# Performance work log

Hardware: AMD Instinct MI355X
Metric: run time of the kernel (lower is better)

The kernel has to match this reference:

```python
import jax, jax.numpy as jnp
from jax import lax
import numpy as np

EPS = 1e-5
K = 16
NUM_GROUP = 128
D = 384
HEADS = 6
DEPTH = 4
BETA = 0.25

def gelu(x):
    return jax.nn.gelu(x, approximate=False)

def linear(x, w, b):
    return x @ w.T + b

def layer_norm(x, g, b):
    mu = x.mean(-1, keepdims=True)
    var = x.var(-1, keepdims=True)
    return (x - mu) / jnp.sqrt(var + EPS) * g + b

def group_norm(x, gamma, beta, groups):
    B, C = x.shape[0], x.shape[1]
    sp = x.shape[2:]
    xg = x.reshape((B, groups, C // groups) + sp)
    axes = tuple(range(2, xg.ndim))
    mu = xg.mean(axes, keepdims=True)
    var = xg.var(axes, keepdims=True)
    xg = (xg - mu) / jnp.sqrt(var + EPS)
    x = xg.reshape((B, C) + sp)
    shp = (1, C) + (1,) * len(sp)
    return x * gamma.reshape(shp) + beta.reshape(shp)

def knn_idx(q, kp, k):
    # q [B,Nq,3], kp [B,Nk,3] -> idx [B,Nq,k] of k nearest keys
    d = jnp.sum(q * q, -1)[:, :, None] - 2.0 * jnp.einsum('bqd,bkd->bqk', q, kp) + jnp.sum(kp * kp, -1)[:, None, :]
    _, idx = lax.top_k(-d, k)
    return idx

def graph_feature(coor_q, x_q, coor_k, x_k, k):
    # coor [B,3,N], x [B,C,N] -> [B,2C,Nq,k]
    idx = knn_idx(coor_q.transpose(0, 2, 1), coor_k.transpose(0, 2, 1), k)
    feat = jax.vmap(lambda a, i: a[:, i])(x_k, idx)  # [B,C,Nq,k]
    xq = x_q[:, :, :, None]
    return jnp.concatenate([feat - xq, jnp.broadcast_to(xq, feat.shape)], axis=1)

def fps_indices(xyz, m):
    # farthest point sampling, start at index 0 (matches pointnet2)
    B, N, _ = xyz.shape
    def body(carry, _):
        dist, far = carry
        c = jnp.take_along_axis(xyz, far[:, None, None], axis=1)
        d = jnp.sum((xyz - c) ** 2, -1)
        dist = jnp.minimum(dist, d)
        return (dist, jnp.argmax(dist, -1).astype(jnp.int32)), far
    init = (jnp.full((B, N), 1e10, xyz.dtype), jnp.zeros((B,), jnp.int32))
    _, idxs = lax.scan(body, init, None, length=m)
    return idxs.T  # [B,m]

def gather_ch(x, idx):
    return jax.vmap(lambda a, i: a[:, i])(x, idx)

def conv1x1_2d(x, w):
    return jnp.einsum('oc,bcnk->bonk', w, x)

def conv1x1_1d(x, w, b):
    return jnp.einsum('oc,bcn->bon', w, x) + b[None, :, None]

def linear_resize(x, out_len):
    # F.interpolate(mode='linear', align_corners=False) along axis 1 of [B,N,D]
    n = x.shape[1]
    pos = (jnp.arange(out_len, dtype=x.dtype) + 0.5) * (n / out_len) - 0.5
    pos = jnp.clip(pos, 0.0, n - 1.0)
    i0 = jnp.floor(pos).astype(jnp.int32)
    i1 = jnp.minimum(i0 + 1, n - 1)
    w = (pos - i0.astype(x.dtype))[None, :, None]
    return x[:, i0] * (1.0 - w) + x[:, i1] * w

def vq(z, cb, beta):
    d = jnp.sum(z * z, -1, keepdims=True) - 2.0 * (z @ cb.T) + jnp.sum(cb * cb, -1)
    eidx = jnp.argmin(d, -1)
    q = cb[eidx]
    loss = jnp.mean((lax.stop_gradient(z) - q) ** 2) + beta * jnp.mean((z - lax.stop_gradient(q)) ** 2)
    q_st = z + lax.stop_gradient(q - z)  # straight-through
    return q_st, loss, eidx

def forward_core(xyz, it_w, it_b, g1_w, g1_g, g1_bt, g2_w, g2_g, g2_bt, g3_w, g3_g, g3_bt, g4_w, g4_g, g4_bt, pe_w1, pe_b1, pe_w2, pe_b2, ip_w1, ip_b1, ip_w2, ip_b2, ln1_g, ln1_b, qkv_w, qkv_b, o_w, o_b, ln2_g, ln2_b, m1_w, m1_b, m2_w, m2_b, pyr_w1, pyr_b1, pyr_g1, pyr_bt1, pyr_w2, pyr_b2, pyr_g2, pyr_bt2, fus_w, fus_b, cb0, cb1, cb2):
    B = xyz.shape[0]
    x = xyz.transpose(0, 2, 1)  # [B,7,N]
    coor, normal, plane = x[:, :3], x[:, 3:6], x[:, 6:7]
    f = conv1x1_1d(coor, it_w, it_b)  # [B,8,N]

    def edge_conv(cq, fq, ck, fk, w, g, bt, groups):
        h = graph_feature(cq, fq, ck, fk, K)
        h = conv1x1_2d(h, w)
        h = group_norm(h, g, bt, groups)
        h = jnp.where(h > 0, h, 0.2 * h)  # LeakyReLU(0.2)
        return h.max(axis=-1)

    f = edge_conv(coor, f, coor, f, g1_w, g1_g, g1_bt, 4)  # [B,32,N]
    idx = fps_indices(coor.transpose(0, 2, 1), NUM_GROUP)
    coor_q, normal_q, plane_q, f_q = gather_ch(coor, idx), gather_ch(normal, idx), gather_ch(plane, idx), gather_ch(f, idx)
    f = edge_conv(coor_q, f_q, coor, f, g2_w, g2_g, g2_bt, 4)  # [B,64,128]
    coor, normal, plane = coor_q, normal_q, plane_q
    f = edge_conv(coor, f, coor, f, g3_w, g3_g, g3_bt, 4)  # [B,64,128]
    idx = fps_indices(coor.transpose(0, 2, 1), NUM_GROUP)
    coor_q, normal_q, plane_q, f_q = gather_ch(coor, idx), gather_ch(normal, idx), gather_ch(plane, idx), gather_ch(f, idx)
    f = edge_conv(coor_q, f_q, coor, f, g4_w, g4_g, g4_bt, 4)  # [B,128,128]
    coor = coor_q.transpose(0, 2, 1)  # [B,128,3]
    f = f.transpose(0, 2, 1)          # [B,128,128]

    pe = linear(gelu(linear(coor, pe_w1, pe_b1)), pe_w2, pe_b2)
    h = linear(gelu(linear(f, ip_w1, ip_b1)), ip_w2, ip_b2)
    t = h + pe
    hd = D // HEADS
    scale = 1.0 / np.sqrt(hd)
    N = t.shape[1]
    for l in range(DEPTH):
        hn = layer_norm(t, ln1_g[l], ln1_b[l])
        qkv = hn @ qkv_w[l] + qkv_b[l]
        q, k_, v = jnp.split(qkv, 3, axis=-1)
        q = q.reshape(B, N, HEADS, hd)
        k_ = k_.reshape(B, N, HEADS, hd)
        v = v.reshape(B, N, HEADS, hd)
        att = jax.nn.softmax(jnp.einsum('bqhd,bkhd->bhqk', q, k_) * scale, axis=-1)
        o = jnp.einsum('bhqk,bkhd->bqhd', att, v).reshape(B, N, D)
        t = t + o @ o_w[l] + o_b[l]
        hn = layer_norm(t, ln2_g[l], ln2_b[l])
        t = t + gelu(hn @ m1_w[l] + m1_b[l]) @ m2_w[l] + m2_b[l]

    base = t  # [B,128,384]
    cbs = (cb0, cb1, cb2)
    outs, losses, idxs = [], [], []
    prev = None
    for level in range(3):
        res = max(base.shape[1] // (2 ** level), 8)
        if res == base.shape[1]:
            lf = base
        else:
            # adaptive_avg_pool1d with evenly dividing bins == reshape-mean
            lf = base.reshape(B, res, base.shape[1] // res, D).mean(2)
        c = lf.transpose(0, 2, 1)
        c = gelu(group_norm(conv1x1_1d(c, pyr_w1[level], pyr_b1[level]), pyr_g1[level], pyr_bt1[level], 8))
        c = gelu(group_norm(conv1x1_1d(c, pyr_w2[level], pyr_b2[level]), pyr_g2[level], pyr_bt2[level], 8))
        proc = c.transpose(0, 2, 1)
        if level > 0:
            pu = prev if prev.shape[1] == res else linear_resize(prev, res)
            proc = gelu(linear(jnp.concatenate([proc, pu], axis=-1), fus_w[level - 1], fus_b[level - 1]))
        q_st, loss, eidx = vq(proc, cbs[level], BETA)
        outs.append(q_st)
        losses.append(loss)
        idxs.append(eidx)
        prev = q_st
    return outs, losses, idxs

def setup_inputs():
    key = jax.random.key(0)
    cnt = [0]
    def nrm(shape, s=0.02):
        cnt[0] += 1
        return jax.random.normal(jax.random.fold_in(key, cnt[0]), shape, jnp.float32) * s
    L = 4
    inp = {}
    inp['xyz'] = nrm((8, 4096, 7), 1.0)
    inp['it_w'] = nrm((8, 3), 0.3)
    inp['it_b'] = jnp.zeros((8,), jnp.float32)
    inp['g1_w'] = nrm((32, 16), 0.1); inp['g1_g'] = jnp.ones((32,)); inp['g1_bt'] = jnp.zeros((32,))
    inp['g2_w'] = nrm((64, 64), 0.1); inp['g2_g'] = jnp.ones((64,)); inp['g2_bt'] = jnp.zeros((64,))
    inp['g3_w'] = nrm((64, 128), 0.1); inp['g3_g'] = jnp.ones((64,)); inp['g3_bt'] = jnp.zeros((64,))
    inp['g4_w'] = nrm((128, 128), 0.1); inp['g4_g'] = jnp.ones((128,)); inp['g4_bt'] = jnp.zeros((128,))
    inp['pe_w1'] = nrm((128, 3), 0.3); inp['pe_b1'] = jnp.zeros((128,))
    inp['pe_w2'] = nrm((D, 128), 0.05); inp['pe_b2'] = jnp.zeros((D,))
    inp['ip_w1'] = nrm((512, 128), 0.05); inp['ip_b1'] = jnp.zeros((512,))
    inp['ip_w2'] = nrm((D, 512), 0.03); inp['ip_b2'] = jnp.zeros((D,))
    inp['ln1_g'] = jnp.ones((L, D)); inp['ln1_b'] = jnp.zeros((L, D))
    inp['qkv_w'] = nrm((L, D, 3 * D)); inp['qkv_b'] = jnp.zeros((L, 3 * D))
    inp['o_w'] = nrm((L, D, D)); inp['o_b'] = jnp.zeros((L, D))
    inp['ln2_g'] = jnp.ones((L, D)); inp['ln2_b'] = jnp.zeros((L, D))
    inp['m1_w'] = nrm((L, D, 4 * D)); inp['m1_b'] = jnp.zeros((L, 4 * D))
    inp['m2_w'] = nrm((L, 4 * D, D)); inp['m2_b'] = jnp.zeros((L, D))
    inp['pyr_w1'] = nrm((3, 2 * D, D), 0.03); inp['pyr_b1'] = jnp.zeros((3, 2 * D))
    inp['pyr_g1'] = jnp.ones((3, 2 * D)); inp['pyr_bt1'] = jnp.zeros((3, 2 * D))
    inp['pyr_w2'] = nrm((3, D, 2 * D), 0.03); inp['pyr_b2'] = jnp.zeros((3, D))
    inp['pyr_g2'] = jnp.ones((3, D)); inp['pyr_bt2'] = jnp.zeros((3, D))
    inp['fus_w'] = nrm((2, D, 2 * D), 0.03); inp['fus_b'] = jnp.zeros((2, D))
    inp['cb0'] = nrm((8192, D), 0.5)
    inp['cb1'] = nrm((4096, D), 0.5)
    inp['cb2'] = nrm((2048, D), 0.5)
    return inp

def reference(xyz, it_w, it_b, g1_w, g1_g, g1_bt, g2_w, g2_g, g2_bt, g3_w, g3_g, g3_bt, g4_w, g4_g, g4_bt, pe_w1, pe_b1, pe_w2, pe_b2, ip_w1, ip_b1, ip_w2, ip_b2, ln1_g, ln1_b, qkv_w, qkv_b, o_w, o_b, ln2_g, ln2_b, m1_w, m1_b, m2_w, m2_b, pyr_w1, pyr_b1, pyr_g1, pyr_bt1, pyr_w2, pyr_b2, pyr_g2, pyr_bt2, fus_w, fus_b, cb0, cb1, cb2):
    outs, losses, idxs = forward_core(xyz, it_w, it_b, g1_w, g1_g, g1_bt, g2_w, g2_g, g2_bt, g3_w, g3_g, g3_bt, g4_w, g4_g, g4_bt, pe_w1, pe_b1, pe_w2, pe_b2, ip_w1, ip_b1, ip_w2, ip_b2, ln1_g, ln1_b, qkv_w, qkv_b, o_w, o_b, ln2_g, ln2_b, m1_w, m1_b, m2_w, m2_b, pyr_w1, pyr_b1, pyr_g1, pyr_bt1, pyr_w2, pyr_b2, pyr_g2, pyr_bt2, fus_w, fus_b, cb0, cb1, cb2)
    # concat quantized features of the 3 levels (128+64+32 tokens), total VQ loss, per-level indices
    return (jnp.concatenate(outs, axis=1), losses[0] + losses[1] + losses[2], idxs[0], idxs[1], idxs[2])
```

## Files before the change

### kernel.cpp

```cpp
#include <hip/hip_runtime.h>
#include <math.h>

#define EPSF 1e-5f

__device__ __forceinline__ float geluf(float x){
  return 0.5f*x*(1.0f + erff(x*0.70710678118654752440f));
}

typedef __attribute__((ext_vector_type(8))) short bf16x8;
typedef __attribute__((ext_vector_type(4))) float f32x4;

__device__ __forceinline__ void split_rne(float x, short& h, short& l){
  union{float f; unsigned u;} xu; xu.f = x;
  unsigned lsb = (xu.u >> 16) & 1u;
  unsigned hb = (xu.u + 0x7fffu + lsb) >> 16;
  union{unsigned u; float f;} hf; hf.u = hb << 16;
  float lof = x - hf.f;
  union{float f; unsigned u;} lu; lu.f = lof;
  unsigned lsb2 = (lu.u >> 16) & 1u;
  unsigned lb = (lu.u + 0x7fffu + lsb2) >> 16;
  h = (short)hb;
  l = (short)lb;
}


__global__ void extract_coor(const float* __restrict__ xyz, float* __restrict__ coor, int B, int N){
  int i = blockIdx.x*blockDim.x + threadIdx.x;
  if(i >= B*3*N) return;
  int n = i % N; int c = (i/N)%3; int b = i/(3*N);
  coor[i] = xyz[((size_t)b*N + n)*7 + c];
}

__global__ void init_feat(const float* __restrict__ xyz, const float* __restrict__ w,
                          const float* __restrict__ bias, float* __restrict__ f, int B, int N){
  int i = blockIdx.x*blockDim.x + threadIdx.x;
  if(i >= B*8*N) return;
  int n = i % N; int c = (i/N)%8; int b = i/(8*N);
  const float* p = xyz + ((size_t)b*N + n)*7;
  f[i] = w[c*3+0]*p[0] + w[c*3+1]*p[1] + w[c*3+2]*p[2] + bias[c];
}

__global__ void transpose_cn(const float* __restrict__ src, float* __restrict__ dst, int B, int C, int N){
  int i = blockIdx.x*blockDim.x + threadIdx.x;
  if(i >= B*C*N) return;
  int c = i % C; int n = (i/C)%N; int b = i/(C*N);
  dst[i] = src[((size_t)b*C + c)*N + n];
}

__global__ void gather_ch_kernel(const float* __restrict__ src, const int* __restrict__ idx,
                                 float* __restrict__ dst, int B, int C, int N, int M){
  int i = blockIdx.x*blockDim.x + threadIdx.x;
  if(i >= B*C*M) return;
  int m = i % M; int c = (i/M)%C; int b = i/(C*M);
  dst[i] = src[((size_t)b*C + c)*N + idx[b*M + m]];
// ... 2 lines not shown
__global__ void split_planes(const float* __restrict__ src, short* __restrict__ hi,
                             short* __restrict__ lo, int n4){
  int i = blockIdx.x*blockDim.x + threadIdx.x;
  if(i >= n4) return;
  float4 v = *(const float4*)(src + (size_t)i*4);
  short h0,h1,h2,h3,l0,l1,l2,l3;
  split_rne(v.x,h0,l0); split_rne(v.y,h1,l1); split_rne(v.z,h2,l2); split_rne(v.w,h3,l3);
  unsigned hw0 = ((unsigned)(unsigned short)h0) | (((unsigned)(unsigned short)h1)<<16);
  unsigned hw1 = ((unsigned)(unsigned short)h2) | (((unsigned)(unsigned short)h3)<<16);
  unsigned lw0 = ((unsigned)(unsigned short)l0) | (((unsigned)(unsigned short)l1)<<16);
  unsigned lw1 = ((unsigned)(unsigned short)l2) | (((unsigned)(unsigned short)l3)<<16);
  ((unsigned*)hi)[(size_t)i*2+0] = hw0; ((unsigned*)hi)[(size_t)i*2+1] = hw1;
  ((unsigned*)lo)[(size_t)i*2+0] = lw0; ((unsigned*)lo)[(size_t)i*2+1] = lw1;
}

#define KNN_K 16
template<int NKMAX, int NT>
__global__ __launch_bounds__(NT) void knn_kernel(const float* __restrict__ Q, const float* __restrict__ Kp,
                                                 int* __restrict__ idxout, int B, int Nq, int Nk){
  constexpr int NW = NT/64;
  __shared__ float4 sk[NKMAX];
  __shared__ float scd[NW][64];
  __shared__ int   sci[NW][64];
  __shared__ int   scnt[NW];
  int qi0 = blockIdx.x*NW;
  int b = qi0 / Nq;
  const float* kb = Kp + (size_t)b*3*Nk;
  if(threadIdx.x < NW) scnt[threadIdx.x] = 0;
  for(int n=threadIdx.x; n<Nk; n+=NT){
    float x = kb[n], y = kb[Nk+n], z = kb[2*Nk+n];
    sk[n] = make_float4(x, y, z, fmaf(x,x, fmaf(y,y, z*z)));
  }
  __syncthreads();
  int wave = threadIdx.x >> 6;
  int lane = threadIdx.x & 63;
  int n_q = qi0 + wave - b*Nq;
  float nqx = -2.0f*Q[((size_t)b*3+0)*Nq + n_q];
  float nqy = -2.0f*Q[((size_t)b*3+1)*Nq + n_q];
  float nqz = -2.0f*Q[((size_t)b*3+2)*Nq + n_q];

  float mind = INFINITY;
  for(int n=lane; n<Nk; n+=64){
    float4 k4 = sk[n];
    float d = fmaf(nqx, k4.x, fmaf(nqy, k4.y, fmaf(nqz, k4.z, k4.w)));
    mind = fminf(mind, d);
  }
  {
    float v = mind;
    #pragma unroll
    for(int k=2;k<=64;k<<=1){
      #pragma unroll
      for(int j=k>>1;j>=1;j>>=1){
        float ov = __shfl_xor(v, j, 64);
        bool lower = (lane & j)==0;
        bool asc = (lane & k)==0;
        float mn = fminf(v,ov), mx = fmaxf(v,ov);
        v = (lower==asc) ? mn : mx;
      }
    }
    mind = v;
  }
  float tau = __shfl(mind, 15, 64);

  for(int n=lane; n<Nk; n+=64){
    float4 k4 = sk[n];
    float d = fmaf(nqx, k4.x, fmaf(nqy, k4.y, fmaf(nqz, k4.z, k4.w)));
    if(d <= tau){
      int slot = atomicAdd(&scnt[wave], 1);
      if(slot < 64){ scd[wave][slot] = d; sci[wave][slot] = n; }
    }
  }
  __syncthreads();
  int cnt = scnt[wave];

  int* orow = idxout + ((size_t)b*Nq + n_q)*KNN_K;
  if(cnt <= 64){
    float d = (lane < cnt) ? scd[wave][lane] : INFINITY;
    int  id = (lane < cnt) ? sci[wave][lane] : 0x7fffffff;
    #pragma unroll
    for(int k=2;k<=64;k<<=1){
      #pragma unroll
      for(int j=k>>1;j>=1;j>>=1){
        float od = __shfl_xor(d, j, 64);
        int oi = __shfl_xor(id, j, 64);
        bool lower = (lane & j)==0;
        bool asc = (lane & k)==0;
        bool otherSmaller = (od < d) || (od==d && oi < id);
        if((lower==asc) == otherSmaller){ d = od; id = oi; }
      }
    }
    if(lane < KNN_K) orow[lane] = id;
  } else {
    float bd[KNN_K]; int bi2[KNN_K];
    #pragma unroll
    for(int j=0;j<KNN_K;j++){ bd[j]=INFINITY; bi2[j]=0x7fffffff; }
    float curmax = INFINITY;
    for(int n=lane; n<Nk; n+=64){
      float4 k4 = sk[n];
      float d = fmaf(nqx, k4.x, fmaf(nqy, k4.y, fmaf(nqz, k4.z, k4.w)));
      if(d < curmax){
        int pm = 0; float md = bd[0]; int mi = bi2[0];
        #pragma unroll
        for(int j=1;j<KNN_K;j++){
          if(bd[j] > md || (bd[j]==md && bi2[j] > mi)){ md=bd[j]; mi=bi2[j]; pm=j; }
        }
        #pragma unroll
        for(int j=0;j<KNN_K;j++){ if(j==pm){ bd[j]=d; bi2[j]=n; } }
        float m2 = -INFINITY;
        #pragma unroll
        for(int j=0;j<KNN_K;j++) m2 = fmaxf(m2, bd[j]);
        curmax = m2;
      }
    }
    for(int t=0;t<KNN_K;t++){
      float ld = bd[0]; int li_ = bi2[0];
      #pragma unroll
      for(int j=1;j<KNN_K;j++){
        if(bd[j] < ld || (bd[j]==ld && bi2[j] < li_)){ ld=bd[j]; li_=bi2[j]; }
      }
      float wd = ld; int wi = li_;
      #pragma unroll
      for(int m=1;m<64;m<<=1){
        float od = __shfl_xor(wd, m, 64);
        int oi = __shfl_xor(wi, m, 64);
        if(od < wd || (od==wd && oi < wi)){ wd=od; wi=oi; }
      }
      if(ld==wd && li_==wi){
        #pragma unroll
        for(int j=0;j<KNN_K;j++){ if(bd[j]==wd && bi2[j]==wi){ bd[j]=INFINITY; bi2[j]=0x7fffffff; } }
      }
      if(lane==0) orow[t] = wi;
    }
  }
}

template<int NMAX, int PPT, int NT>
__global__ __launch_bounds__(NT) void fps_kernel(const float* __restrict__ coor, int* __restrict__ out,
                                                 int N, int M){
  __shared__ float skx[NMAX], sky[NMAX], skz[NMAX];
  __shared__ unsigned long long swk[NT/64];
  __shared__ int gidx;
  constexpr int NW = NT/64;
  int b = blockIdx.x;
  int tid = threadIdx.x;
  int lane = tid & 63, wid = tid >> 6;
  const float* cx = coor + (size_t)b*3*N;
// ... 299 lines not shown
    }
  };
  auto stageB = [&](){
    #pragma unroll
    for(int v8=0; v8<2; v8++){
      bf16x8 h, l;
      #pragma unroll
      for(int j=0;j<8;j++){
        short th, tl;
        split_rne(breg[v8*8+j], th, tl);
        h[j] = th; l[j] = tl;
      }
      *(bf16x8*)&sBhi[bc_][bkq + v8*8] = h;
      *(bf16x8*)&sBlo[bc_][bkq + v8*8] = l;
    }
  };

  loadA(0); loadB(0);
  int nk = K >> 6;
  for(int ki=0; ki<nk; ki++){
    stageA(ki*64); stageB();
    __syncthreads();
    if(ki+1 < nk){ loadA((ki+1)*64); loadB((ki+1)*64); }
    #pragma unroll
    for(int half=0; half<2; half++){
      bf16x8 ah[2], al[2], bh[2], bl[2];
      #pragma unroll
      for(int m=0;m<2;m++){
        int arow = wm*32 + m*16 + rr;
        ah[m] = *(bf16x8*)&sAhi[arow][half*32 + g*8];
// ... 269 lines not shown
  }
}

__global__ void loss_kernel(const float* __restrict__ lossacc, float* __restrict__ out){
  float m0 = lossacc[0]/(8.0f*128.0f*384.0f);
  float m1 = lossacc[1]/(8.0f*64.0f*384.0f);
  float m2 = lossacc[2]/(8.0f*32.0f*384.0f);
  out[0] = (m0 + 0.25f*m0) + (m1 + 0.25f*m1) + (m2 + 0.25f*m2);
}


extern "C" void kernel_launch(void* const* d_in, const int* in_sizes, int n_in,
                              void* d_out, int out_size, void* d_ws, size_t ws_size,
                              hipStream_t stream)
{
  (void)in_sizes; (void)n_in; (void)out_size; (void)ws_size;
  const float* xyz   = (const float*)d_in[0];
  const float* it_w  = (const float*)d_in[1];
  const float* it_b  = (const float*)d_in[2];
  const float* g1_w  = (const float*)d_in[3];
  const float* g1_g  = (const float*)d_in[4];
  const float* g1_bt = (const float*)d_in[5];
  const float* g2_w  = (const float*)d_in[6];
  const float* g2_g  = (const float*)d_in[7];
  const float* g2_bt = (const float*)d_in[8];
  const float* g3_w  = (const float*)d_in[9];
  const float* g3_g  = (const float*)d_in[10];
  const float* g3_bt = (const float*)d_in[11];
  const float* g4_w  = (const float*)d_in[12];
  const float* g4_g  = (const float*)d_in[13];
  const float* g4_bt = (const float*)d_in[14];
// ... 61 lines not shown
  constexpr size_t OFF_LF    = OFF_MID + (size_t)1024*1536;
  constexpr size_t OFF_C1    = OFF_LF + (size_t)512*384;
  constexpr size_t OFF_C2    = OFF_C1 + (size_t)1024*768;
  constexpr size_t OFF_CAT   = OFF_C2 + (size_t)1024*384;
  constexpr size_t OFF_PROC  = OFF_CAT + (size_t)512*768;
  constexpr size_t OFF_KEYS  = OFF_PROC + (size_t)512*384;
  constexpr size_t OFF_LNMR  = OFF_KEYS + 3584;
  constexpr size_t OFF_CBSQ  = OFF_LNMR + 2048;
  constexpr size_t OFF_PART  = OFF_CBSQ + 14336;
  constexpr size_t OFF_MR    = OFF_PART + 32768;
  constexpr size_t OFF_LOSS  = OFF_MR + 64;
  constexpr size_t OFF_ZHI   = OFF_LOSS + 64;
  constexpr size_t OFF_ZLO   = OFF_ZHI + 196608;
  constexpr size_t OFF_CBHI  = OFF_ZLO + 196608;
  constexpr size_t OFF_CBLO  = OFF_CBHI + 2752512;

  float* coor0 = ws + OFF_COOR0;
  float* f0    = ws + OFF_F0;
  float* f1    = ws + OFF_F1;
  int*   idx1  = (int*)(ws + OFF_IDX1);
  int*   fps1  = (int*)(ws + OFF_FPS1);
  float* coor1 = ws + OFF_COOR1;
  float* f1q   = ws + OFF_F1Q;
  int*   idx2  = (int*)(ws + OFF_IDX2);
  float* f2    = ws + OFF_F2;
  int*   idx3  = (int*)(ws + OFF_IDX3);
  float* f3    = ws + OFF_F3;
  int*   fps2  = (int*)(ws + OFF_FPS2);
  float* coor2 = ws + OFF_COOR2;
  float* f3q   = ws + OFF_F3Q;
// ... 9 lines not shown
  float* lfb   = ws + OFF_LF;
  float* c1b   = ws + OFF_C1;
  float* c2b   = ws + OFF_C2;
  float* catb  = ws + OFF_CAT;
  float* procb = ws + OFF_PROC;
  unsigned long long* keys = (unsigned long long*)(ws + OFF_KEYS);
  float* lnst  = ws + OFF_LNMR;
  float* cbsq  = ws + OFF_CBSQ;
  float* part  = ws + OFF_PART;
  float* mr    = ws + OFF_MR;
  float* lossa = ws + OFF_LOSS;
  short* zhi   = (short*)(ws + OFF_ZHI);
  short* zlo   = (short*)(ws + OFF_ZLO);
  short* cbhi  = (short*)(ws + OFF_CBHI);
  short* cblo  = (short*)(ws + OFF_CBLO);

  auto cdiv = [](int a, int b){ return (a+b-1)/b; };
  auto gemm_full = [&](const float* A, const float* Bm, const float* bias, float* C,
                       int M, int N, int K, int BT, int act, int addto,
                       const float* lnmr, const float* lng, const float* lnb){
    if(((K & 63) == 0) && ((N & 63) == 0) && ((M & 63) == 0)){
      dim3 g(N/64, M/64);
      gemm_mfma<<<g, 256, 0, stream>>>(A, Bm, bias, C, M, N, K, BT, act, addto, lnmr, lng, lnb);
    } else {
      dim3 g(N/64, M/64), blk(128);
      gemm64<<<g, blk, 0, stream>>>(A, Bm, bias, C, M, N, K, BT, act, addto);
    }
  };
  auto gemm = [&](const float* A, const float* Bm, const float* bias, float* C,
                  int M, int N, int K, int BT, int act, int addto){
    gemm_full(A, Bm, bias, C, M, N, K, BT, act, addto, nullptr, nullptr, nullptr);
  };

  hipMemsetAsync(lossa, 0, 8*sizeof(float), stream);
  hipMemsetAsync(keys, 0xFF, 1792*sizeof(unsigned long long), stream);

  extract_coor<<<cdiv(B_*3*N0,256),256,0,stream>>>(xyz, coor0, B_, N0);
  init_feat<<<cdiv(B_*8*N0,256),256,0,stream>>>(xyz, it_w, it_b, f0, B_, N0);

  split_planes<<<cdiv(8192*384/4,256),256,0,stream>>>(cb0, cbhi, cblo, 8192*384/4);
  split_planes<<<cdiv(4096*384/4,256),256,0,stream>>>(cb1, cbhi + (size_t)8192*384, cblo + (size_t)8192*384, 4096*384/4);
  split_planes<<<cdiv(2048*384/4,256),256,0,stream>>>(cb2, cbhi + (size_t)12288*384, cblo + (size_t)12288*384, 2048*384/4);
  cbsq_kernel<<<cdiv(8192,256),256,0,stream>>>(cb0, cbsq, 8192);
  cbsq_kernel<<<cdiv(4096,256),256,0,stream>>>(cb1, cbsq+8192, 4096);
  cbsq_kernel<<<cdiv(2048,256),256,0,stream>>>(cb2, cbsq+12288, 2048);

  knn_kernel<4096,512><<<B_*N0/8,512,0,stream>>>(coor0, coor0, idx1, B_, N0, N0);
  ec_main<8,32><<<B_*32*N0/256,256,0,stream>>>(f0, f0, idx1, g1_w, f1, part, N0, N0);
  ec_reduce<<<32,256,0,stream>>>(part, mr, 32*N0/256, 1.0f/(8.0f*N0*16.0f));
  ec_norm<<<cdiv(B_*32*N0,256),256,0,stream>>>(f1, mr, g1_g, g1_bt, N0, 32, B_*32*N0);

  fps_kernel<4096,8,512><<<B_,512,0,stream>>>(coor0, fps1, N0, M0);
  gather_ch_kernel<<<cdiv(B_*3*M0,256),256,0,stream>>>(coor0, fps1, coor1, B_, 3, N0, M0);
  gather_ch_kernel<<<cdiv(B_*32*M0,256),256,0,stream>>>(f1, fps1, f1q, B_, 32, N0, M0);

  knn_kernel<4096,512><<<B_*M0/8,512,0,stream>>>(coor1, coor0, idx2, B_, M0, N0);
  ec_main<32,64><<<B_*64*M0/256,256,0,stream>>>(f1q, f1, idx2, g2_w, f2, part, M0, N0);
  ec_reduce<<<32,256,0,stream>>>(part, mr, 64*M0/256, 1.0f/(16.0f*M0*16.0f));
  ec_norm<<<cdiv(B_*64*M0,256),256,0,stream>>>(f2, mr, g2_g, g2_bt, M0, 64, B_*64*M0);

  knn_kernel<128,512><<<B_*M0/8,512,0,stream>>>(coor1, coor1, idx3, B_, M0, M0);
  ec_main<64,64><<<B_*64*M0/256,256,0,stream>>>(f2, f2, idx3, g3_w, f3, part, M0, M0);
  ec_reduce<<<32,256,0,stream>>>(part, mr, 64*M0/256, 1.0f/(16.0f*M0*16.0f));
  ec_norm<<<cdiv(B_*64*M0,256),256,0,stream>>>(f3, mr, g3_g, g3_bt, M0, 64, B_*64*M0);

  fps_kernel<128,1,128><<<B_,128,0,stream>>>(coor1, fps2, M0, M0);
  gather_ch_kernel<<<cdiv(B_*3*M0,256),256,0,stream>>>(coor1, fps2, coor2, B_, 3, M0, M0);
  gather_ch_kernel<<<cdiv(B_*64*M0,256),256,0,stream>>>(f3, fps2, f3q, B_, 64, M0, M0);

  knn_kernel<128,512><<<B_*M0/8,512,0,stream>>>(coor2, coor1, idx4, B_, M0, M0);
  ec_main<64,128><<<B_*128*M0/256,256,0,stream>>>(f3q, f3, idx4, g4_w, f4, part, M0, M0);
  ec_reduce<<<32,256,0,stream>>>(part, mr, 128*M0/256, 1.0f/(32.0f*M0*16.0f));
  ec_norm<<<cdiv(B_*128*M0,256),256,0,stream>>>(f4, mr, g4_g, g4_bt, M0, 128, B_*128*M0);

  transpose_cn<<<cdiv(B_*3*M0,256),256,0,stream>>>(coor2, coorT, B_, 3, M0);
  transpose_cn<<<cdiv(B_*128*M0,256),256,0,stream>>>(f4, fT, B_, 128, M0);

  gemm(coorT, pe_w1, pe_b1, tmp, 1024, 128, 3, 1, 1, 0);
  gemm(tmp, pe_w2, pe_b2, tbuf, 1024, 384, 128, 1, 0, 0);
  gemm(fT, ip_w1, ip_b1, tmp, 1024, 512, 128, 1, 1, 0);
  gemm(tmp, ip_w2, ip_b2, tbuf, 1024, 384, 512, 1, 0, 1);

  for(int l=0;l<4;l++){
    ln_stats<<<256,256,0,stream>>>(tbuf, lnst, 384);
    gemm_full(tbuf, qkv_w + (size_t)l*384*1152, qkv_b + l*1152, qkvb, 1024, 1152, 384, 0, 0, 0,
              lnst, ln1_g + l*384, ln1_b + l*384);
    attn_kernel<<<48,128,0,stream>>>(qkvb, attb);
    gemm(attb, o_w + (size_t)l*384*384, o_b + l*384, tbuf, 1024, 384, 384, 0, 0, 1);
    ln_stats<<<256,256,0,stream>>>(tbuf, lnst, 384);
    gemm_full(tbuf, m1_w + (size_t)l*384*1536, m1_b + l*1536, midb, 1024, 1536, 384, 0, 1, 0,
              lnst, ln2_g + l*384, ln2_b + l*384);
    gemm(midb, m2_w + (size_t)l*1536*384, m2_b + l*384, tbuf, 1024, 384, 1536, 0, 0, 1);
  }

  const float* cbs[3] = {cb0, cb1, cb2};
  const int ncodes[3] = {8192, 4096, 2048};
  const int cboff[3]  = {0, 8192, 12288};
  const int keyoff[3] = {0, 1024, 1536};
  const int rowoffs[3] = {0, 128, 192};
  const size_t OUT0 = (size_t)8*224*384;
  float* idxouts[3] = { out + OUT0 + 1, out + OUT0 + 1 + 1024, out + OUT0 + 1 + 1536 };

  for(int lv=0; lv<3; ++lv){
    int res = 128 >> lv;
    int rows = 8*res;
    const float* lf;
    if(lv==0){ lf = tbuf; }
    else {
      pool_kernel<<<cdiv(rows*384,256),256,0,stream>>>(tbuf, lfb, B_, res, 1<<lv);
      lf = lfb;
    }
    gemm(lf, pyr_w1 + (size_t)lv*768*384, pyr_b1 + lv*768, c1b, rows, 768, 384, 1, 0, 0);
    gn_gelu_kernel<<<64,256,0,stream>>>(c1b, pyr_g1 + lv*768, pyr_bt1 + lv*768, res, 768, 96);
    gemm(c1b, pyr_w2 + (size_t)lv*384*768, pyr_b2 + lv*384, c2b, rows, 384, 768, 1, 0, 0);
    gn_gelu_kernel<<<64,256,0,stream>>>(c2b, pyr_g2 + lv*384, pyr_bt2 + lv*384, res, 384, 48);
    const float* z = c2b;
    if(lv > 0){
      pu_cat_kernel<<<cdiv(rows*768,256),256,0,stream>>>(c2b, out, catb, B_, res, rowoffs[lv-1]);
      gemm(catb, fus_w + (size_t)(lv-1)*384*768, fus_b + (lv-1)*384, procb, rows, 384, 768, 1, 1, 0);
      z = procb;
    }
    split_planes<<<cdiv(rows*384/4,256),256,0,stream>>>(z, zhi, zlo, rows*384/4);
    gemm_vq<<<dim3(ncodes[lv]/64, rows/64), 256, 0, stream>>>(zhi, zlo,
        cbhi + (size_t)cboff[lv]*384, cblo + (size_t)cboff[lv]*384,
        cbsq + cboff[lv], keys + keyoff[lv], rows, ncodes[lv], 384);
    vq_out_kernel<<<rows,128,0,stream>>>(z, keys + keyoff[lv], cbs[lv], out, lossa + lv, res,
                                         rowoffs[lv], idxouts[lv]);
  }

  loss_kernel<<<1,1,0,stream>>>(lossa, out + OUT0);
}
```

Measured before the change: 1.813 ms.

## Pre-split weights into bf16 hi/lo planes, pair kNN queries per wave, fuse init kernels

All dense weights are transposed and split once per call into bf16 hi/lo planes in the workspace. A new MFMA GEMM then reads these planes directly instead of converting fp32 weights inside every tile. The kNN kernel now handles two queries per wave so each shared-memory key read serves two distance computations. The coordinate-extract and initial-feature kernels are merged into one launch. The price is extra preprocessing launches and workspace on every call, with a fallback to the old GEMM path when the workspace is too small.

```diff
diff --git a/kernel.cpp b/kernel.cpp
--- a/kernel.cpp
+++ b/kernel.cpp
@@ -24,20 +24,20 @@
 }
 
 
-__global__ void extract_coor(const float* __restrict__ xyz, float* __restrict__ coor, int B, int N){
+__global__ void init_pts(const float* __restrict__ xyz, const float* __restrict__ w,
+                         const float* __restrict__ bias, float* __restrict__ coor,
+                         float* __restrict__ f, int B, int N){
   int i = blockIdx.x*blockDim.x + threadIdx.x;
-  if(i >= B*3*N) return;
-  int n = i % N; int c = (i/N)%3; int b = i/(3*N);
-  coor[i] = xyz[((size_t)b*N + n)*7 + c];
-}
-
-__global__ void init_feat(const float* __restrict__ xyz, const float* __restrict__ w,
-                          const float* __restrict__ bias, float* __restrict__ f, int B, int N){
-  int i = blockIdx.x*blockDim.x + threadIdx.x;
-  if(i >= B*8*N) return;
-  int n = i % N; int c = (i/N)%8; int b = i/(8*N);
-  const float* p = xyz + ((size_t)b*N + n)*7;
-  f[i] = w[c*3+0]*p[0] + w[c*3+1]*p[1] + w[c*3+2]*p[2] + bias[c];
+  if(i >= B*N) return;
+  int n = i % N; int b = i / N;
+  const float* p = xyz + (size_t)i*7;
+  float x = p[0], y = p[1], z = p[2];
+  coor[((size_t)b*3+0)*N+n] = x;
+  coor[((size_t)b*3+1)*N+n] = y;
+  coor[((size_t)b*3+2)*N+n] = z;
+  #pragma unroll
+  for(int c=0;c<8;c++)
+    f[((size_t)b*8+c)*N+n] = w[c*3+0]*x + w[c*3+1]*y + w[c*3+2]*z + bias[c];
 }
 
 __global__ void transpose_cn(const float* __restrict__ src, float* __restrict__ dst, int B, int C, int N){
@@ -70,19 +70,40 @@
   ((unsigned*)lo)[(size_t)i*2+0] = lw0; ((unsigned*)lo)[(size_t)i*2+1] = lw1;
 }
 
+__global__ __launch_bounds__(256) void transpose_split(const float* __restrict__ src,
+    short* __restrict__ hi, short* __restrict__ lo, int K, int N){
+  __shared__ float tile[32][33];
+  int bn = blockIdx.x*32, bk = blockIdx.y*32;
+  int tx = threadIdx.x & 31, ty = threadIdx.x >> 5;
+  #pragma unroll
+  for(int i=ty; i<32; i+=8){
+    int k = bk+i, n = bn+tx;
+    tile[i][tx] = (k<K && n<N) ? src[(size_t)k*N+n] : 0.f;
+  }
+  __syncthreads();
+  #pragma unroll
+  for(int i=ty; i<32; i+=8){
+    int n = bn+i, k = bk+tx;
+    if(n<N && k<K){
+      short h,l; split_rne(tile[tx][i], h, l);
+      hi[(size_t)n*K+k] = h; lo[(size_t)n*K+k] = l;
+    }
+  }
+}
+
 #define KNN_K 16
 template<int NKMAX, int NT>
-__global__ __launch_bounds__(NT) void knn_kernel(const float* __restrict__ Q, const float* __restrict__ Kp,
-                                                 int* __restrict__ idxout, int B, int Nq, int Nk){
+__global__ __launch_bounds__(NT) void knn2q_kernel(const float* __restrict__ Q, const float* __restrict__ Kp,
+                                                   int* __restrict__ idxout, int B, int Nq, int Nk){
   constexpr int NW = NT/64;
   __shared__ float4 sk[NKMAX];
-  __shared__ float scd[NW][64];
-  __shared__ int   sci[NW][64];
-  __shared__ int   scnt[NW];
-  int qi0 = blockIdx.x*NW;
-  int b = qi0 / Nq;
+  __shared__ float scd[NW][2][64];
+  __shared__ int   sci[NW][2][64];
+  __shared__ int   scnt[NW][2];
+  int qb = blockIdx.x*(NW*2);
+  int b = qb / Nq;
   const float* kb = Kp + (size_t)b*3*Nk;
-  if(threadIdx.x < NW) scnt[threadIdx.x] = 0;
+  if(threadIdx.x < NW*2) ((int*)scnt)[threadIdx.x] = 0;
   for(int n=threadIdx.x; n<Nk; n+=NT){
     float x = kb[n], y = kb[Nk+n], z = kb[2*Nk+n];
     sk[n] = make_float4(x, y, z, fmaf(x,x, fmaf(y,y, z*z)));
@@ -90,102 +111,119 @@
   __syncthreads();
   int wave = threadIdx.x >> 6;
   int lane = threadIdx.x & 63;
-  int n_q = qi0 + wave - b*Nq;
-  float nqx = -2.0f*Q[((size_t)b*3+0)*Nq + n_q];
-  float nqy = -2.0f*Q[((size_t)b*3+1)*Nq + n_q];
-  float nqz = -2.0f*Q[((size_t)b*3+2)*Nq + n_q];
-
-  float mind = INFINITY;
+  int nq0 = qb + wave*2 - b*Nq;
+  float q0x = -2.0f*Q[((size_t)b*3+0)*Nq + nq0];
+  float q0y = -2.0f*Q[((size_t)b*3+1)*Nq + nq0];
+  float q0z = -2.0f*Q[((size_t)b*3+2)*Nq + nq0];
+  float q1x = -2.0f*Q[((size_t)b*3+0)*Nq + nq0+1];
+  float q1y = -2.0f*Q[((size_t)b*3+1)*Nq + nq0+1];
+  float q1z = -2.0f*Q[((size_t)b*3+2)*Nq + nq0+1];
+
+  float mind0 = INFINITY, mind1 = INFINITY;
   for(int n=lane; n<Nk; n+=64){
     float4 k4 = sk[n];
-    float d = fmaf(nqx, k4.x, fmaf(nqy, k4.y, fmaf(nqz, k4.z, k4.w)));
-    mind = fminf(mind, d);
+    float d0 = fmaf(q0x, k4.x, fmaf(q0y, k4.y, fmaf(q0z, k4.z, k4.w)));
+    float d1 = fmaf(q1x, k4.x, fmaf(q1y, k4.y, fmaf(q1z, k4.z, k4.w)));
+    mind0 = fminf(mind0, d0);
+    mind1 = fminf(mind1, d1);
   }
   {
-    float v = mind;
+    float v0 = mind0, v1 = mind1;
     #pragma unroll
     for(int k=2;k<=64;k<<=1){
       #pragma unroll
       for(int j=k>>1;j>=1;j>>=1){
-        float ov = __shfl_xor(v, j, 64);
-        bool lower = (lane & j)==0;
-        bool asc = (lane & k)==0;
-        float mn = fminf(v,ov), mx = fmaxf(v,ov);
-        v = (lower==asc) ? mn : mx;
-      }
-    }
-    mind = v;
-  }
-  float tau = __shfl(mind, 15, 64);
+        float o0 = __shfl_xor(v0, j, 64);
+        float o1 = __shfl_xor(v1, j, 64);
+        bool keepmin = ((lane & j)==0) == ((lane & k)==0);
+        v0 = keepmin ? fminf(v0,o0) : fmaxf(v0,o0);
+        v1 = keepmin ? fminf(v1,o1) : fmaxf(v1,o1);
+      }
+    }
+    mind0 = v0; mind1 = v1;
+  }
+  float tau0 = __shfl(mind0, 15, 64);
+  float tau1 = __shfl(mind1, 15, 64);
 
   for(int n=lane; n<Nk; n+=64){
     float4 k4 = sk[n];
-    float d = fmaf(nqx, k4.x, fmaf(nqy, k4.y, fmaf(nqz, k4.z, k4.w)));
-    if(d <= tau){
-      int slot = atomicAdd(&scnt[wave], 1);
-      if(slot < 64){ scd[wave][slot] = d; sci[wave][slot] = n; }
+    float d0 = fmaf(q0x, k4.x, fmaf(q0y, k4.y, fmaf(q0z, k4.z, k4.w)));
+    float d1 = fmaf(q1x, k4.x, fmaf(q1y, k4.y, fmaf(q1z, k4.z, k4.w)));
+    if(d0 <= tau0){
+      int slot = atomicAdd(&scnt[wave][0], 1);
+      if(slot < 64){ scd[wave][0][slot] = d0; sci[wave][0][slot] = n; }
+    }
+    if(d1 <= tau1){
+      int slot = atomicAdd(&scnt[wave][1], 1);
+      if(slot < 64){ scd[wave][1][slot] = d1; sci[wave][1][slot] = n; }
     }
   }
   __syncthreads();
-  int cnt = scnt[wave];
-
-  int* orow = idxout + ((size_t)b*Nq + n_q)*KNN_K;
-  if(cnt <= 64){
-    float d = (lane < cnt) ? scd[wave][lane] : INFINITY;
-    int  id = (lane < cnt) ? sci[wave][lane] : 0x7fffffff;
-    #pragma unroll
-    for(int k=2;k<=64;k<<=1){
-      #pragma unroll
-      for(int j=k>>1;j>=1;j>>=1){
-        float od = __shfl_xor(d, j, 64);
-        int oi = __shfl_xor(id, j, 64);
-        bool lower = (lane & j)==0;
-        bool asc = (lane & k)==0;
-        bool otherSmaller = (od < d) || (od==d && oi < id);
-        if((lower==asc) == otherSmaller){ d = od; id = oi; }
-      }
-    }
-    if(lane < KNN_K) orow[lane] = id;
-  } else {
-    float bd[KNN_K]; int bi2[KNN_K];
-    #pragma unroll
-    for(int j=0;j<KNN_K;j++){ bd[j]=INFINITY; bi2[j]=0x7fffffff; }
-    float curmax = INFINITY;
-    for(int n=lane; n<Nk; n+=64){
-      float4 k4 = sk[n];
-      float d = fmaf(nqx, k4.x, fmaf(nqy, k4.y, fmaf(nqz, k4.z, k4.w)));
-      if(d < curmax){
-        int pm = 0; float md = bd[0]; int mi = bi2[0];
+
+  #pragma unroll
+  for(int qq=0; qq<2; qq++){
+    int cnt = scnt[wave][qq];
+    int* orow = idxout + ((size_t)b*Nq + nq0 + qq)*KNN_K;
+    float nqx = qq ? q1x : q0x;
+    float nqy = qq ? q1y : q0y;
+    float nqz = qq ? q1z : q0z;
+    if(cnt <= 64){
+      float d = (lane < cnt) ? scd[wave][qq][lane] : INFINITY;
+      int  id = (lane < cnt) ? sci[wave][qq][lane] : 0x7fffffff;
+      #pragma unroll
+      for(int k=2;k<=64;k<<=1){
+        #pragma unroll
+        for(int j=k>>1;j>=1;j>>=1){
+          float od = __shfl_xor(d, j, 64);
+          int oi = __shfl_xor(id, j, 64);
+          bool lower = (lane & j)==0;
+          bool asc = (lane & k)==0;
+          bool otherSmaller = (od < d) || (od==d && oi < id);
+          if((lower==asc) == otherSmaller){ d = od; id = oi; }
+        }
+      }
+      if(lane < KNN_K) orow[lane] = id;
+    } else {
+      float bd[KNN_K]; int bi2[KNN_K];
+      #pragma unroll
+      for(int j=0;j<KNN_K;j++){ bd[j]=INFINITY; bi2[j]=0x7fffffff; }
+      float curmax = INFINITY;
+      for(int n=lane; n<Nk; n+=64){
+        float4 k4 = sk[n];
+        float d = fmaf(nqx, k4.x, fmaf(nqy, k4.y, fmaf(nqz, k4.z, k4.w)));
+        if(d < curmax){
+          int pm = 0; float md = bd[0]; int mi = bi2[0];
+          #pragma unroll
+          for(int j=1;j<KNN_K;j++){
+            if(bd[j] > md || (bd[j]==md && bi2[j] > mi)){ md=bd[j]; mi=bi2[j]; pm=j; }
+          }
+          #pragma unroll
+          for(int j=0;j<KNN_K;j++){ if(j==pm){ bd[j]=d; bi2[j]=n; } }
+          float m2 = -INFINITY;
+          #pragma unroll
+          for(int j=0;j<KNN_K;j++) m2 = fmaxf(m2, bd[j]);
+          curmax = m2;
+        }
+      }
+      for(int t=0;t<KNN_K;t++){
+        float ld = bd[0]; int li_ = bi2[0];
         #pragma unroll
         for(int j=1;j<KNN_K;j++){
-          if(bd[j] > md || (bd[j]==md && bi2[j] > mi)){ md=bd[j]; mi=bi2[j]; pm=j; }
+          if(bd[j] < ld || (bd[j]==ld && bi2[j] < li_)){ ld=bd[j]; li_=bi2[j]; }
         }
+        float wd = ld; int wi = li_;
         #pragma unroll
-        for(int j=0;j<KNN_K;j++){ if(j==pm){ bd[j]=d; bi2[j]=n; } }
-        float m2 = -INFINITY;
-        #pragma unroll
-        for(int j=0;j<KNN_K;j++) m2 = fmaxf(m2, bd[j]);
-        curmax = m2;
-      }
-    }
-    for(int t=0;t<KNN_K;t++){
-      float ld = bd[0]; int li_ = bi2[0];
-      #pragma unroll
-      for(int j=1;j<KNN_K;j++){
-        if(bd[j] < ld || (bd[j]==ld && bi2[j] < li_)){ ld=bd[j]; li_=bi2[j]; }
-      }
-      float wd = ld; int wi = li_;
-      #pragma unroll
-      for(int m=1;m<64;m<<=1){
-        float od = __shfl_xor(wd, m, 64);
-        int oi = __shfl_xor(wi, m, 64);
-        if(od < wd || (od==wd && oi < wi)){ wd=od; wi=oi; }
-      }
-      if(ld==wd && li_==wi){
-        #pragma unroll
-        for(int j=0;j<KNN_K;j++){ if(bd[j]==wd && bi2[j]==wi){ bd[j]=INFINITY; bi2[j]=0x7fffffff; } }
-      }
-      if(lane==0) orow[t] = wi;
+        for(int m=1;m<64;m<<=1){
+          float od = __shfl_xor(wd, m, 64);
+          int oi = __shfl_xor(wi, m, 64);
+          if(od < wd || (od==wd && oi < wi)){ wd=od; wi=oi; }
+        }
+        if(ld==wd && li_==wi){
+          #pragma unroll
+          for(int j=0;j<KNN_K;j++){ if(bd[j]==wd && bi2[j]==wi){ bd[j]=INFINITY; bi2[j]=0x7fffffff; } }
+        }
+        if(lane==0) orow[t] = wi;
+      }
     }
   }
 }
@@ -515,6 +553,126 @@
       *(bf16x8*)&sBhi[bc_][bkq + v8*8] = h;
       *(bf16x8*)&sBlo[bc_][bkq + v8*8] = l;
     }
+  };
+
+  loadA(0); loadB(0);
+  int nk = K >> 6;
+  for(int ki=0; ki<nk; ki++){
+    stageA(ki*64); stageB();
+    __syncthreads();
+    if(ki+1 < nk){ loadA((ki+1)*64); loadB((ki+1)*64); }
+    #pragma unroll
+    for(int half=0; half<2; half++){
+      bf16x8 ah[2], al[2], bh[2], bl[2];
+      #pragma unroll
+      for(int m=0;m<2;m++){
+        int arow = wm*32 + m*16 + rr;
+        ah[m] = *(bf16x8*)&sAhi[arow][half*32 + g*8];
+        al[m] = *(bf16x8*)&sAlo[arow][half*32 + g*8];
+      }
+      #pragma unroll
+      for(int n=0;n<2;n++){
+        int bcol = wn*32 + n*16 + rr;
+        bh[n] = *(bf16x8*)&sBhi[bcol][half*32 + g*8];
+        bl[n] = *(bf16x8*)&sBlo[bcol][half*32 + g*8];
+      }
+      #pragma unroll
+      for(int m=0;m<2;m++){
+        #pragma unroll
+        for(int n=0;n<2;n++){
+          acc[m][n] = __builtin_amdgcn_mfma_f32_16x16x32_bf16(ah[m], bh[n], acc[m][n], 0, 0, 0);
+          acc[m][n] = __builtin_amdgcn_mfma_f32_16x16x32_bf16(ah[m], bl[n], acc[m][n], 0, 0, 0);
+          acc[m][n] = __builtin_amdgcn_mfma_f32_16x16x32_bf16(al[m], bh[n], acc[m][n], 0, 0, 0);
+        }
+      }
+    }
+    __syncthreads();
+  }
+  #pragma unroll
+  for(int n=0;n<2;n++){
+    int col = bn + wn*32 + n*16 + rr;
+    float bb = bias ? bias[col] : 0.f;
+    #pragma unroll
+    for(int m=0;m<2;m++){
+      #pragma unroll
+      for(int r4=0;r4<4;r4++){
+        int row = bm + wm*32 + m*16 + g*4 + r4;
+        float v = acc[m][n][r4] + bb;
+        if(act==1) v = geluf(v);
+        size_t o = (size_t)row*N + col;
+        if(addto) v += C[o];
+        C[o] = v;
+      }
+    }
+  }
+}
+
+__global__ __launch_bounds__(256) void gemm_mfma_ps(const float* __restrict__ A,
+    const short* __restrict__ Bhi, const short* __restrict__ Blo,
+    const float* __restrict__ bias, float* __restrict__ C,
+    int M, int N, int K, int act, int addto,
+    const float* __restrict__ lnmr, const float* __restrict__ lng, const float* __restrict__ lnb)
+{
+  __shared__ short sAhi[64][72];
+  __shared__ short sAlo[64][72];
+  __shared__ short sBhi[64][72];
+  __shared__ short sBlo[64][72];
+  int t = threadIdx.x;
+  int lane = t & 63, wave = t >> 6;
+  int wm = wave >> 1, wn = wave & 1;
+  int g = lane >> 4, rr = lane & 15;
+  int bm = blockIdx.y*64, bn = blockIdx.x*64;
+  f32x4 acc[2][2];
+  #pragma unroll
+  for(int m=0;m<2;m++)
+    #pragma unroll
+    for(int n=0;n<2;n++)
+      #pragma unroll
+      for(int r=0;r<4;r++) acc[m][n][r] = 0.f;
+
+  int ar_ = t >> 2, akq = (t & 3)*16;
+  float lmu = 0.f, lrstd = 0.f;
+  if(lnmr){ lmu = lnmr[(bm+ar_)*2+0]; lrstd = lnmr[(bm+ar_)*2+1]; }
+
+  float areg[16];
+  bf16x8 pbh[2], pbl[2];
+  auto loadA = [&](int k0){
+    const float* ap = A + (size_t)(bm + ar_)*K + k0 + akq;
+    *(float4*)&areg[0]  = *(const float4*)(ap);
+    *(float4*)&areg[4]  = *(const float4*)(ap+4);
+    *(float4*)&areg[8]  = *(const float4*)(ap+8);
+    *(float4*)&areg[12] = *(const float4*)(ap+12);
+  };
+  auto loadB = [&](int k0){
+    const short* hp = Bhi + (size_t)(bn + ar_)*K + k0 + akq;
+    const short* lp = Blo + (size_t)(bn + ar_)*K + k0 + akq;
+    pbh[0] = *(const bf16x8*)hp; pbh[1] = *(const bf16x8*)(hp+8);
+    pbl[0] = *(const bf16x8*)lp; pbl[1] = *(const bf16x8*)(lp+8);
+  };
+  auto stageA = [&](int k0){
+    #pragma unroll
+    for(int v8=0; v8<2; v8++){
+      bf16x8 h, l;
+      #pragma unroll
+      for(int j=0;j<8;j++){
+        float x = areg[v8*8+j];
+        if(lnmr){
+          int kk = k0 + akq + v8*8 + j;
+          x = (x - lmu)*lrstd*lng[kk] + lnb[kk];
+        }
+        short th, tl;
+        split_rne(x, th, tl);
+        h[j] = th; l[j] = tl;
+      }
+      *(bf16x8*)&sAhi[ar_][akq + v8*8] = h;
+      *(bf16x8*)&sAlo[ar_][akq + v8*8] = l;
+    }
+  };
+  auto stageB = [&](){
+    *(bf16x8*)&sBhi[ar_][akq]   = pbh[0];
+    *(bf16x8*)&sBhi[ar_][akq+8] = pbh[1];
+    *(bf16x8*)&sBlo[ar_][akq]   = pbl[0];
+    *(bf16x8*)&sBlo[ar_][akq+8] = pbl[1];
   };
 
   loadA(0); loadB(0);
@@ -814,7 +972,7 @@
                               void* d_out, int out_size, void* d_ws, size_t ws_size,
                               hipStream_t stream)
 {
-  (void)in_sizes; (void)n_in; (void)out_size; (void)ws_size;
+  (void)in_sizes; (void)n_in; (void)out_size;
   const float* xyz   = (const float*)d_in[0];
   const float* it_w  = (const float*)d_in[1];
   const float* it_b  = (const float*)d_in[2];
@@ -906,6 +1064,20 @@
   constexpr size_t OFF_ZLO   = OFF_ZHI + 196608;
   constexpr size_t OFF_CBHI  = OFF_ZLO + 196608;
   constexpr size_t OFF_CBLO  = OFF_CBHI + 2752512;
+  constexpr size_t WQKV = 0;
+  constexpr size_t WO   = WQKV + (size_t)4*1152*384;
+  constexpr size_t WM1  = WO   + (size_t)4*384*384;
+  constexpr size_t WM2  = WM1  + (size_t)4*1536*384;
+  constexpr size_t WIP1 = WM2  + (size_t)4*384*1536;
+  constexpr size_t WIP2 = WIP1 + (size_t)512*128;
+  constexpr size_t WPE2 = WIP2 + (size_t)384*512;
+  constexpr size_t WPY1 = WPE2 + (size_t)384*128;
+  constexpr size_t WPY2 = WPY1 + (size_t)3*768*384;
+  constexpr size_t WFUS = WPY2 + (size_t)3*384*768;
+  constexpr size_t WTOT = WFUS + (size_t)2*384*768;
+  constexpr size_t OFF_WHI = OFF_CBLO + 2752512;
+  constexpr size_t OFF_WLO = OFF_WHI + (WTOT+1)/2;
+  constexpr size_t OFF_END = OFF_WLO + (WTOT+1)/2;
 
   float* coor0 = ws + OFF_COOR0;
   float* f0    = ws + OFF_F0;
@@ -945,6 +1117,10 @@
   short* zlo   = (short*)(ws + OFF_ZLO);
   short* cbhi  = (short*)(ws + OFF_CBHI);
   short* cblo  = (short*)(ws + OFF_CBLO);
+  short* whi   = (short*)(ws + OFF_WHI);
+  short* wlo   = (short*)(ws + OFF_WLO);
+
+  bool presplit = ws_size >= OFF_END * sizeof(float);
 
   auto cdiv = [](int a, int b){ return (a+b-1)/b; };
   auto gemm_full = [&](const float* A, const float* Bm, const float* bias, float* C,
@@ -958,16 +1134,21 @@
       gemm64<<<g, blk, 0, stream>>>(A, Bm, bias, C, M, N, K, BT, act, addto);
     }
   };
-  auto gemm = [&](const float* A, const float* Bm, const float* bias, float* C,
-                  int M, int N, int K, int BT, int act, int addto){
-    gemm_full(A, Bm, bias, C, M, N, K, BT, act, addto, nullptr, nullptr, nullptr);
+  auto gemmW = [&](const float* A, const float* W, size_t wofs, const float* bias, float* C,
+                   int M, int N, int K, int BT, int act, int addto,
+                   const float* lnmr, const float* lng, const float* lnb){
+    if(presplit && ((K & 63) == 0) && ((N & 63) == 0) && ((M & 63) == 0)){
+      dim3 g(N/64, M/64);
+      gemm_mfma_ps<<<g, 256, 0, stream>>>(A, whi + wofs, wlo + wofs, bias, C, M, N, K, act, addto, lnmr, lng, lnb);
+    } else {
+      gemm_full(A, W, bias, C, M, N, K, BT, act, addto, lnmr, lng, lnb);
+    }
   };
 
   hipMemsetAsync(lossa, 0, 8*sizeof(float), stream);
   hipMemsetAsync(keys, 0xFF, 1792*sizeof(unsigned long long), stream);
 
-  extract_coor<<<cdiv(B_*3*N0,256),256,0,stream>>>(xyz, coor0, B_, N0);
-  init_feat<<<cdiv(B_*8*N0,256),256,0,stream>>>(xyz, it_w, it_b, f0, B_, N0);
+  init_pts<<<cdiv(B_*N0,256),256,0,stream>>>(xyz, it_w, it_b, coor0, f0, B_, N0);
 
   split_planes<<<cdiv(8192*384/4,256),256,0,stream>>>(cb0, cbhi, cblo, 8192*384/4);
   split_planes<<<cdiv(4096*384/4,256),256,0,stream>>>(cb1, cbhi + (size_t)8192*384, cblo + (size_t)8192*384, 4096*384/4);
@@ -976,7 +1157,26 @@
   cbsq_kernel<<<cdiv(4096,256),256,0,stream>>>(cb1, cbsq+8192, 4096);
   cbsq_kernel<<<cdiv(2048,256),256,0,stream>>>(cb2, cbsq+12288, 2048);
 
-  knn_kernel<4096,512><<<B_*N0/8,512,0,stream>>>(coor0, coor0, idx1, B_, N0, N0);
+  if(presplit){
+    for(int l=0;l<4;l++){
+      transpose_split<<<dim3(1152/32,384/32),256,0,stream>>>(qkv_w + (size_t)l*384*1152,
+          whi + WQKV + (size_t)l*1152*384, wlo + WQKV + (size_t)l*1152*384, 384, 1152);
+      transpose_split<<<dim3(384/32,384/32),256,0,stream>>>(o_w + (size_t)l*384*384,
+          whi + WO + (size_t)l*384*384, wlo + WO + (size_t)l*384*384, 384, 384);
+      transpose_split<<<dim3(1536/32,384/32),256,0,stream>>>(m1_w + (size_t)l*384*1536,
+          whi + WM1 + (size_t)l*1536*384, wlo + WM1 + (size_t)l*1536*384, 384, 1536);
+      transpose_split<<<dim3(384/32,1536/32),256,0,stream>>>(m2_w + (size_t)l*1536*384,
+          whi + WM2 + (size_t)l*384*1536, wlo + WM2 + (size_t)l*384*1536, 1536, 384);
+    }
+    split_planes<<<cdiv(512*128/4,256),256,0,stream>>>(ip_w1, whi+WIP1, wlo+WIP1, 512*128/4);
+    split_planes<<<cdiv(384*512/4,256),256,0,stream>>>(ip_w2, whi+WIP2, wlo+WIP2, 384*512/4);
+    split_planes<<<cdiv(384*128/4,256),256,0,stream>>>(pe_w2, whi+WPE2, wlo+WPE2, 384*128/4);
+    split_planes<<<cdiv(3*768*384/4,256),256,0,stream>>>(pyr_w1, whi+WPY1, wlo+WPY1, 3*768*384/4);
+    split_planes<<<cdiv(3*384*768/4,256),256,0,stream>>>(pyr_w2, whi+WPY2, wlo+WPY2, 3*384*768/4);
+    split_planes<<<cdiv(2*384*768/4,256),256,0,stream>>>(fus_w, whi+WFUS, wlo+WFUS, 2*384*768/4);
+  }
+
+  knn2q_kernel<4096,512><<<B_*N0/16,512,0,stream>>>(coor0, coor0, idx1, B_, N0, N0);
   ec_main<8,32><<<B_*32*N0/256,256,0,stream>>>(f0, f0, idx1, g1_w, f1, part, N0, N0);
   ec_reduce<<<32,256,0,stream>>>(part, mr, 32*N0/256, 1.0f/(8.0f*N0*16.0f));
   ec_norm<<<cdiv(B_*32*N0,256),256,0,stream>>>(f1, mr, g1_g, g1_bt, N0, 32, B_*32*N0);
@@ -985,12 +1185,12 @@
   gather_ch_kernel<<<cdiv(B_*3*M0,256),256,0,stream>>>(coor0, fps1, coor1, B_, 3, N0, M0);
   gather_ch_kernel<<<cdiv(B_*32*M0,256),256,0,stream>>>(f1, fps1, f1q, B_, 32, N0, M0);
 
-  knn_kernel<4096,512><<<B_*M0/8,512,0,stream>>>(coor1, coor0, idx2, B_, M0, N0);
+  knn2q_kernel<4096,512><<<B_*M0/16,512,0,stream>>>(coor1, coor0, idx2, B_, M0, N0);
   ec_main<32,64><<<B_*64*M0/256,256,0,stream>>>(f1q, f1, idx2, g2_w, f2, part, M0, N0);
   ec_reduce<<<32,256,0,stream>>>(part, mr, 64*M0/256, 1.0f/(16.0f*M0*16.0f));
   ec_norm<<<cdiv(B_*64*M0,256),256,0,stream>>>(f2, mr, g2_g, g2_bt, M0, 64, B_*64*M0);
 
-  knn_kernel<128,512><<<B_*M0/8,512,0,stream>>>(coor1, coor1, idx3, B_, M0, M0);
+  knn2q_kernel<128,512><<<B_*M0/16,512,0,stream>>>(coor1, coor1, idx3, B_, M0, M0);
   ec_main<64,64><<<B_*64*M0/256,256,0,stream>>>(f2, f2, idx3, g3_w, f3, part, M0, M0);
   ec_reduce<<<32,256,0,stream>>>(part, mr, 64*M0/256, 1.0f/(16.0f*M0*16.0f));
   ec_norm<<<cdiv(B_*64*M0,256),256,0,stream>>>(f3, mr, g3_g, g3_bt, M0, 64, B_*64*M0);
@@ -999,7 +1199,7 @@
   gather_ch_kernel<<<cdiv(B_*3*M0,256),256,0,stream>>>(coor1, fps2, coor2, B_, 3, M0, M0);
   gather_ch_kernel<<<cdiv(B_*64*M0,256),256,0,stream>>>(f3, fps2, f3q, B_, 64, M0, M0);
 
-  knn_kernel<128,512><<<B_*M0/8,512,0,stream>>>(coor2, coor1, idx4, B_, M0, M0);
+  knn2q_kernel<128,512><<<B_*M0/16,512,0,stream>>>(coor2, coor1, idx4, B_, M0, M0);
   ec_main<64,128><<<B_*128*M0/256,256,0,stream>>>(f3q, f3, idx4, g4_w, f4, part, M0, M0);
   ec_reduce<<<32,256,0,stream>>>(part, mr, 128*M0/256, 1.0f/(32.0f*M0*16.0f));
   ec_norm<<<cdiv(B_*128*M0,256),256,0,stream>>>(f4, mr, g4_g, g4_bt, M0, 128, B_*128*M0);
@@ -1007,21 +1207,23 @@
   transpose_cn<<<cdiv(B_*3*M0,256),256,0,stream>>>(coor2, coorT, B_, 3, M0);
   transpose_cn<<<cdiv(B_*128*M0,256),256,0,stream>>>(f4, fT, B_, 128, M0);
 
-  gemm(coorT, pe_w1, pe_b1, tmp, 1024, 128, 3, 1, 1, 0);
-  gemm(tmp, pe_w2, pe_b2, tbuf, 1024, 384, 128, 1, 0, 0);
-  gemm(fT, ip_w1, ip_b1, tmp, 1024, 512, 128, 1, 1, 0);
-  gemm(tmp, ip_w2, ip_b2, tbuf, 1024, 384, 512, 1, 0, 1);
+  gemm_full(coorT, pe_w1, pe_b1, tmp, 1024, 128, 3, 1, 1, 0, nullptr, nullptr, nullptr);
+  gemmW(tmp, pe_w2, WPE2, pe_b2, tbuf, 1024, 384, 128, 1, 0, 0, nullptr, nullptr, nullptr);
+  gemmW(fT, ip_w1, WIP1, ip_b1, tmp, 1024, 512, 128, 1, 1, 0, nullptr, nullptr, nullptr);
+  gemmW(tmp, ip_w2, WIP2, ip_b2, tbuf, 1024, 384, 512, 1, 0, 1, nullptr, nullptr, nullptr);
 
   for(int l=0;l<4;l++){
     ln_stats<<<256,256,0,stream>>>(tbuf, lnst, 384);
-    gemm_full(tbuf, qkv_w + (size_t)l*384*1152, qkv_b + l*1152, qkvb, 1024, 1152, 384, 0, 0, 0,
-              lnst, ln1_g + l*384, ln1_b + l*384);
+    gemmW(tbuf, qkv_w + (size_t)l*384*1152, WQKV + (size_t)l*1152*384, qkv_b + l*1152, qkvb,
+          1024, 1152, 384, 0, 0, 0, lnst, ln1_g + l*384, ln1_b + l*384);
     attn_kernel<<<48,128,0,stream>>>(qkvb, attb);
-    gemm(attb, o_w + (size_t)l*384*384, o_b + l*384, tbuf, 1024, 384, 384, 0, 0, 1);
+    gemmW(attb, o_w + (size_t)l*384*384, WO + (size_t)l*384*384, o_b + l*384, tbuf,
+          1024, 384, 384, 0, 0, 1, nullptr, nullptr, nullptr);
     ln_stats<<<256,256,0,stream>>>(tbuf, lnst, 384);
-    gemm_full(tbuf, m1_w + (size_t)l*384*1536, m1_b + l*1536, midb, 1024, 1536, 384, 0, 1, 0,
-              lnst, ln2_g + l*384, ln2_b + l*384);
-    gemm(midb, m2_w + (size_t)l*1536*384, m2_b + l*384, tbuf, 1024, 384, 1536, 0, 0, 1);
+    gemmW(tbuf, m1_w + (size_t)l*384*1536, WM1 + (size_t)l*1536*384, m1_b + l*1536, midb,
+          1024, 1536, 384, 0, 1, 0, lnst, ln2_g + l*384, ln2_b + l*384);
+    gemmW(midb, m2_w + (size_t)l*1536*384, WM2 + (size_t)l*384*1536, m2_b + l*384, tbuf,
+          1024, 384, 1536, 0, 0, 1, nullptr, nullptr, nullptr);
   }
 
   const float* cbs[3] = {cb0, cb1, cb2};
@@ -1041,14 +1243,17 @@
       pool_kernel<<<cdiv(rows*384,256),256,0,stream>>>(tbuf, lfb, B_, res, 1<<lv);
       lf = lfb;
     }
-    gemm(lf, pyr_w1 + (size_t)lv*768*384, pyr_b1 + lv*768, c1b, rows, 768, 384, 1, 0, 0);
+    gemmW(lf, pyr_w1 + (size_t)lv*768*384, WPY1 + (size_t)lv*768*384, pyr_b1 + lv*768, c1b,
+          rows, 768, 384, 1, 0, 0, nullptr, nullptr, nullptr);
     gn_gelu_kernel<<<64,256,0,stream>>>(c1b, pyr_g1 + lv*768, pyr_bt1 + lv*768, res, 768, 96);
-    gemm(c1b, pyr_w2 + (size_t)lv*384*768, pyr_b2 + lv*384, c2b, rows, 384, 768, 1, 0, 0);
+    gemmW(c1b, pyr_w2 + (size_t)lv*384*768, WPY2 + (size_t)lv*384*768, pyr_b2 + lv*384, c2b,
+          rows, 384, 768, 1, 0, 0, nullptr, nullptr, nullptr);
     gn_gelu_kernel<<<64,256,0,stream>>>(c2b, pyr_g2 + lv*384, pyr_bt2 + lv*384, res, 384, 48);
     const float* z = c2b;
     if(lv > 0){
       pu_cat_kernel<<<cdiv(rows*768,256),256,0,stream>>>(c2b, out, catb, B_, res, rowoffs[lv-1]);
-      gemm(catb, fus_w + (size_t)(lv-1)*384*768, fus_b + (lv-1)*384, procb, rows, 384, 768, 1, 1, 0);
+      gemmW(catb, fus_w + (size_t)(lv-1)*384*768, WFUS + (size_t)(lv-1)*384*768, fus_b + (lv-1)*384, procb,
+            rows, 384, 768, 1, 1, 0, nullptr, nullptr, nullptr);
       z = procb;
     }
     split_planes<<<cdiv(rows*384/4,256),256,0,stream>>>(z, zhi, zlo, rows*384/4);
```

Result: no change. 1.798 ms (-0.9%).
